# Optimization experiments

Hardware: AMD Instinct MI355X
Metric: run time of the kernel (lower is better)

Reference implementation:

```python
import jax, jax.numpy as jnp
import numpy as np

HIDDEN = 1024
HEADS = 16
HEAD_DIM = HIDDEN // HEADS  # 64
MLP_HIDDEN = int(HIDDEN * 4.0)  # 4096
B, L = 2, 2048
EPS_LN = 1e-6
EPS_RMS = 1e-6


def setup_inputs() -> dict:
    key = jax.random.key(0)
    ks = jax.random.split(key, 12)
    s = 0.02
    return {
        "x": jax.random.normal(ks[0], (B, L, HIDDEN), jnp.float32),
        "vec": jax.random.normal(ks[1], (B, HIDDEN), jnp.float32),
        "pe": jax.random.normal(ks[2], (1, 1, L, HEAD_DIM // 2, 2, 2), jnp.float32),
        "w_mod": jax.random.normal(ks[3], (HIDDEN, 3 * HIDDEN), jnp.float32) * s,
        "b_mod": jnp.zeros((3 * HIDDEN,), jnp.float32),
        "w1": jax.random.normal(ks[4], (HIDDEN, 3 * HIDDEN + MLP_HIDDEN), jnp.float32) * s,
        "b1": jnp.zeros((3 * HIDDEN + MLP_HIDDEN,), jnp.float32),
        "w_mlp": jax.random.normal(ks[5], (MLP_HIDDEN, HIDDEN), jnp.float32) * s,
        "b_mlp": jnp.zeros((HIDDEN,), jnp.float32),
        "w2": jax.random.normal(ks[6], (2 * HIDDEN, HIDDEN), jnp.float32) * s,
        "b2": jnp.zeros((HIDDEN,), jnp.float32),
        "q_scale": jnp.ones((HEAD_DIM,), jnp.float32),
        "k_scale": jnp.ones((HEAD_DIM,), jnp.float32),
    }


def _layernorm(x, eps=EPS_LN):
    m = jnp.mean(x, axis=-1, keepdims=True)
    v = jnp.mean(jnp.square(x - m), axis=-1, keepdims=True)
    return (x - m) * jax.lax.rsqrt(v + eps)


def _rmsnorm(x, scale, eps=EPS_RMS):
    rrms = jax.lax.rsqrt(jnp.mean(jnp.square(x), axis=-1, keepdims=True) + eps)
    return x * rrms * scale


def _apply_rope(t, pe):
    # t: [B,H,L,D]; pe: [1,1,L,D//2,2,2]
    t_ = t.reshape(*t.shape[:-1], -1, 1, 2)  # [B,H,L,D//2,1,2]
    out = pe[..., 0] * t_[..., 0] + pe[..., 1] * t_[..., 1]  # [B,H,L,D//2,2]
    return out.reshape(t.shape)


def reference(x, vec, pe, w_mod, b_mod, w1, b1, w_mlp, b_mlp, w2, b2, q_scale, k_scale):
    # adaLN modulation: silu(vec) -> Dense(3*dim) -> shift, scale, gate
    mod = (jax.nn.silu(vec) @ w_mod + b_mod)[:, None, :]  # [B,1,3H]
    shift, scale, gate = jnp.split(mod, 3, axis=-1)
    x_mod = (1.0 + scale) * _layernorm(x) + shift
    # fused QKV + MLP projection
    h = x_mod @ w1 + b1  # [B,L,3H+MH]
    qkv, mlp = h[..., : 3 * HIDDEN], h[..., 3 * HIDDEN :]
    qkv = qkv.reshape(x.shape[0], x.shape[1], 3, HEADS, HEAD_DIM)
    qkv = jnp.transpose(qkv, (2, 0, 3, 1, 4))  # [3,B,H,L,D]
    q, k, v = qkv[0], qkv[1], qkv[2]
    # QK-RMSNorm per head-dim
    q = _rmsnorm(q, q_scale)
    k = _rmsnorm(k, k_scale)
    # RoPE
    q = _apply_rope(q, pe)
    k = _apply_rope(k, pe)
    # attention
    scores = jnp.einsum("bhqd,bhkd->bhqk", q, k) * (HEAD_DIM ** -0.5)
    probs = jax.nn.softmax(scores, axis=-1)
    attn = jnp.einsum("bhqk,bhkd->bhqd", probs, v)
    attn = jnp.transpose(attn, (0, 2, 1, 3)).reshape(x.shape[0], x.shape[1], HIDDEN)
    # mlp branch (Dense with tanh activation per source) + fused output proj
    mlp_out = jnp.tanh(mlp @ w_mlp + b_mlp)
    out = jnp.concatenate([attn, mlp_out], axis=-1) @ w2 + b2
    return x + gate * out
```

## Files before the change

kernel.cpp:

```cpp
#include <hip/hip_runtime.h>
#include <stdint.h>


#define HID  1024
#define NH   16
#define HD   64
#define MLP  4096
#define D1   7168
#define DQKV 3072
#define DCAT 2048
#define BB   2
#define LL   2048
#define TOK  4096

typedef __attribute__((ext_vector_type(8))) short    bf16x8;
typedef __attribute__((ext_vector_type(4))) float    f32x4;
typedef __attribute__((ext_vector_type(4))) unsigned int u32x4;

__device__ __forceinline__ float b2f(unsigned short u) {
    unsigned int v = ((unsigned int)u) << 16;
    float f; __builtin_memcpy(&f, &v, 4); return f;
}
__device__ __forceinline__ unsigned short f2b(float f) {
    unsigned int v; __builtin_memcpy(&v, &f, 4);
    unsigned int r = (v + 0x7FFFu + ((v >> 16) & 1u)) >> 16;
    return (unsigned short)r;
}
__device__ __forceinline__ unsigned int pkbf2(float a, float b) {
    unsigned int ua, ub;
    __builtin_memcpy(&ua, &a, 4); __builtin_memcpy(&ub, &b, 4);
    return ((ua + 0x8000u) >> 16) | ((ub + 0x8000u) & 0xFFFF0000u);
}
__device__ __forceinline__ void gl_lds16(const unsigned short* g, unsigned short* l) {
    __builtin_amdgcn_global_load_lds(
        (const __attribute__((address_space(1))) unsigned int*)(g),
        (__attribute__((address_space(3))) unsigned int*)(l), 16, 0, 0);
}

__global__ void k_transpose_cvt(const float* __restrict__ in,
                                unsigned short* __restrict__ out, int R, int C) {
    __shared__ float tile[32][33];
    int bx = blockIdx.x, by = blockIdx.y;
    int tx = threadIdx.x, ty = threadIdx.y;
    #pragma unroll
    for (int i = 0; i < 4; i++) {
        int r = by * 32 + ty + i * 8;
        int c = bx * 32 + tx;
        tile[ty + i * 8][tx] = in[(size_t)r * C + c];
    }
    __syncthreads();
    #pragma unroll
    for (int i = 0; i < 4; i++) {
        int ro = bx * 32 + ty + i * 8;
        int co = by * 32 + tx;
        out[(size_t)ro * R + co] = f2b(tile[tx][ty + i * 8]);
    }
}

__global__ void k_mod(const float* __restrict__ vec,
                      const float* __restrict__ w_mod,
                      const float* __restrict__ b_mod,
                      float* __restrict__ mod) {
    __shared__ float sv[HID];
    __shared__ float red[8][32];
    int b = blockIdx.y, t = threadIdx.x;
    for (int j = t; j < HID; j += 256) {
        float v = vec[b * HID + j];
        sv[j] = v / (1.0f + __expf(-v));
    }
    __syncthreads();
    int n0 = blockIdx.x * 32;
    int on = t & 31, ks = t >> 5;
    float acc = 0.f;
    const float* wp = w_mod + (size_t)(ks * 128) * 3072 + n0 + on;
    #pragma unroll 4
    for (int k = 0; k < 128; k++) acc += sv[ks * 128 + k] * wp[(size_t)k * 3072];
    red[ks][on] = acc;
    __syncthreads();
    if (t < 32) {
        float s = 0.f;
        #pragma unroll
        for (int i = 0; i < 8; i++) s += red[i][t];
        mod[b * 3072 + n0 + t] = s + b_mod[n0 + t];
    }
}

__global__ void k_lnmod(const float* __restrict__ x,
                        const float* __restrict__ mod,
                        unsigned short* __restrict__ xmod) {
    int tok = blockIdx.x;
    int t = threadIdx.x;
    int b = tok >> 11;
    float4 v4 = *(const float4*)(x + (size_t)tok * HID + t * 4);
    float v0 = v4.x, v1 = v4.y, v2 = v4.z, v3 = v4.w;
    float s  = v0 + v1 + v2 + v3;
    float sq = v0*v0 + v1*v1 + v2*v2 + v3*v3;
    for (int off = 1; off < 64; off <<= 1) {
        s  += __shfl_xor(s,  off);
        sq += __shfl_xor(sq, off);
    }
    __shared__ float ls[4], lq[4];
    int w = t >> 6;
    if ((t & 63) == 0) { ls[w] = s; lq[w] = sq; }
    __syncthreads();
    s  = ls[0] + ls[1] + ls[2] + ls[3];
    sq = lq[0] + lq[1] + lq[2] + lq[3];
    float mean = s * (1.0f / HID);
    float var  = sq * (1.0f / HID) - mean * mean;
    float rstd = rsqrtf(var + 1e-6f);
    const float* mb = mod + b * 3072;
    float y[4] = {v0, v1, v2, v3};
    unsigned short r[4];
    #pragma unroll
    for (int j = 0; j < 4; j++) {
        int col = t * 4 + j;
        float nval = (y[j] - mean) * rstd;
        r[j] = f2b((1.0f + mb[1024 + col]) * nval + mb[col]);
    }
    unsigned int o0 = (unsigned int)r[0] | ((unsigned int)r[1] << 16);
    unsigned int o1 = (unsigned int)r[2] | ((unsigned int)r[3] << 16);
    *(uint2*)(xmod + (size_t)tok * HID + t * 4) = make_uint2(o0, o1);
}

template<int EPI>
__global__ __launch_bounds__(256) void k_gemm(
    const unsigned short* __restrict__ A, int lda,
    const unsigned short* __restrict__ Bt, int ldb,
    const float* __restrict__ bias,
    unsigned short* __restrict__ C, float* __restrict__ Cf, int ldc,
    int K,
    const float* __restrict__ xin,
    const float* __restrict__ mod) {
    __shared__ alignas(16) unsigned short As[128 * 64];
    __shared__ alignas(16) unsigned short Bs[128 * 64];
    int t = threadIdx.x;
    int bm = blockIdx.x, bn = blockIdx.y;
    int lane = t & 63, wave = t >> 6;
    int wm = (wave >> 1) * 64, wn = (wave & 1) * 64;
    int ln = lane & 15, kq = lane >> 4;
    int ln7 = ln & 7;

    f32x4 acc[4][4];
    #pragma unroll
    for (int i = 0; i < 4; i++)
        #pragma unroll
        for (int j = 0; j < 4; j++) acc[i][j] = {0.f, 0.f, 0.f, 0.f};

    int sr  = t >> 3;
    int scg = (t & 7) ^ (sr & 7);
    const unsigned short* Ab = A  + (size_t)(bm * 128) * lda;
    const unsigned short* Bb = Bt + (size_t)(bn * 128) * ldb;

    int ksplit = K / gridDim.z;
    int kbeg = blockIdx.z * ksplit, kend = kbeg + ksplit;

    for (int k0 = kbeg; k0 < kend; k0 += 64) {
        __syncthreads();
        #pragma unroll
        for (int c = 0; c < 4; c++) {
            gl_lds16(Ab + (size_t)(c * 32 + sr) * lda + k0 + scg * 8, &As[c * 2048 + t * 8]);
            gl_lds16(Bb + (size_t)(c * 32 + sr) * ldb + k0 + scg * 8, &Bs[c * 2048 + t * 8]);
        }
        __syncthreads();
        #pragma unroll
        for (int ks = 0; ks < 2; ks++) {
            int slot = ((ks * 4 + kq) ^ ln7) * 8;
            bf16x8 af[4], bfr[4];
            #pragma unroll
            for (int i = 0; i < 4; i++)
                af[i] = *(const bf16x8*)(&As[(wm + i * 16 + ln) * 64 + slot]);
            #pragma unroll
            for (int j = 0; j < 4; j++)
                bfr[j] = *(const bf16x8*)(&Bs[(wn + j * 16 + ln) * 64 + slot]);
            #pragma unroll
            for (int i = 0; i < 4; i++)
                #pragma unroll
                for (int j = 0; j < 4; j++)
                    acc[i][j] = __builtin_amdgcn_mfma_f32_16x16x32_bf16(af[i], bfr[j], acc[i][j], 0, 0, 0);
        }
    }

    #pragma unroll
    for (int i = 0; i < 4; i++) {
        #pragma unroll
        for (int j = 0; j < 4; j++) {
            int col = bn * 128 + wn + j * 16 + ln;
            float bv = (EPI == 3) ? 0.f : bias[col];
            #pragma unroll
            for (int r = 0; r < 4; r++) {
                int row = bm * 128 + wm + i * 16 + kq * 4 + r;
                float v = acc[i][j][r] + bv;
                if (EPI == 0) {
                    C[(size_t)row * ldc + col] = f2b(v);
                } else if (EPI == 1) {
                    C[(size_t)row * ldc + col] = f2b(tanhf(v));
                } else if (EPI == 2) {
                    int b = row >> 11;
                    Cf[(size_t)row * ldc + col] =
                        xin[(size_t)row * HID + col] + mod[b * 3072 + 2048 + col] * v;
                } else {
                    Cf[((size_t)blockIdx.z * TOK + row) * ldc + col] = v;
                }
            }
        }
    }
}

__global__ __launch_bounds__(256) void k_red1(const float* __restrict__ part,
                                              const float* __restrict__ bias,
                                              unsigned short* __restrict__ cat) {
    int idx = blockIdx.x * 256 + threadIdx.x;
    int row = idx >> 8;
    int c4  = (idx & 255) * 4;
    float4 p0 = *(const float4*)(part + (size_t)row * HID + c4);
    float4 p1 = *(const float4*)(part + ((size_t)TOK + row) * HID + c4);
    float4 bv = *(const float4*)(bias + c4);
    float a0 = tanhf(p0.x + p1.x + bv.x);
    float a1 = tanhf(p0.y + p1.y + bv.y);
    float a2 = tanhf(p0.z + p1.z + bv.z);
    float a3 = tanhf(p0.w + p1.w + bv.w);
    *(uint2*)(&cat[(size_t)row * DCAT + HID + c4]) =
        make_uint2(pkbf2(a0, a1), pkbf2(a2, a3));
}

__global__ __launch_bounds__(256) void k_red2(const float* __restrict__ part,
                                              const float* __restrict__ bias,
                                              const float* __restrict__ x,
                                              const float* __restrict__ mod,
                                              float* __restrict__ out) {
    int idx = blockIdx.x * 256 + threadIdx.x;
    int row = idx >> 8;
    int c4  = (idx & 255) * 4;
    int b = row >> 11;
    float4 p0 = *(const float4*)(part + (size_t)row * HID + c4);
    float4 p1 = *(const float4*)(part + ((size_t)TOK + row) * HID + c4);
    float4 bv = *(const float4*)(bias + c4);
    float4 gv = *(const float4*)(mod + b * 3072 + 2048 + c4);
    float4 xv = *(const float4*)(x + (size_t)row * HID + c4);
    float4 o;
    o.x = xv.x + gv.x * (p0.x + p1.x + bv.x);
    o.y = xv.y + gv.y * (p0.y + p1.y + bv.y);
    o.z = xv.z + gv.z * (p0.z + p1.z + bv.z);
    o.w = xv.w + gv.w * (p0.w + p1.w + bv.w);
    *(float4*)(out + (size_t)row * HID + c4) = o;
}

__global__ void k_qkrope(unsigned short* __restrict__ h,
                         const float* __restrict__ pe,
                         const float* __restrict__ q_scale,
                         const float* __restrict__ k_scale) {
    int tok = blockIdx.x;
    int l = tok & (LL - 1);
    int t = threadIdx.x;
    int lane = t & 63, wave = t >> 6;
    int hh = wave * 4 + (lane >> 4);
    int d0 = (lane & 15) * 4;
    unsigned short* row = h + (size_t)tok * D1;
    int i0 = d0 >> 1;
    const float* peb = pe + ((size_t)l * 32 + i0) * 4;
    float4 e0 = *(const float4*)(peb);
    float4 e1 = *(const float4*)(peb + 4);
    #pragma unroll
    for (int qk = 0; qk < 2; qk++) {
        unsigned short* p = row + qk * HID + hh * HD + d0;
        const float* sc = (qk == 0 ? q_scale : k_scale) + d0;
        uint2 qv = *(const uint2*)p;
        float v0 = b2f((unsigned short)(qv.x & 0xFFFF)), v1 = b2f((unsigned short)(qv.x >> 16));
        float v2 = b2f((unsigned short)(qv.y & 0xFFFF)), v3 = b2f((unsigned short)(qv.y >> 16));
        float ssq = v0*v0 + v1*v1 + v2*v2 + v3*v3;
        ssq += __shfl_xor(ssq, 1, 16);
        ssq += __shfl_xor(ssq, 2, 16);
        ssq += __shfl_xor(ssq, 4, 16);
        ssq += __shfl_xor(ssq, 8, 16);
        float rr = rsqrtf(ssq * (1.0f / HD) + 1e-6f);
        if (qk == 0) rr *= 0.18033688011112042f;
        v0 *= rr * sc[0];
        v1 *= rr * sc[1];
        v2 *= rr * sc[2];
        v3 *= rr * sc[3];
        float o0 = e0.x*v0 + e0.y*v1;
        float o1 = e0.z*v0 + e0.w*v1;
        float o2 = e1.x*v2 + e1.y*v3;
        float o3 = e1.z*v2 + e1.w*v3;
        *(uint2*)p = make_uint2(pkbf2(o0, o1), pkbf2(o2, o3));
    }
}

#define KT 64
#define LDP 72
__global__ __launch_bounds__(256) void k_attn(const unsigned short* __restrict__ h,
                                              unsigned short* __restrict__ cat) {
    __shared__ unsigned short Ks[KT * LDP];
    __shared__ unsigned short Vt[HD * LDP];
    __shared__ unsigned short Ps[4 * 16 * LDP];
    int t = threadIdx.x;
    int bx = blockIdx.x;
    int bh = blockIdx.y;
    int b = bh >> 4, hh = bh & 15;
    int lane = t & 63, w = t >> 6;
    int ln = lane & 15, quad = lane >> 4;
    const unsigned short* hb = h + (size_t)b * LL * D1;

    bf16x8 qf[2];
    {
        const unsigned short* qbase = hb + (size_t)(bx * 64 + w * 16) * D1 + hh * HD;
        #pragma unroll
        for (int ks = 0; ks < 2; ks++)
            qf[ks] = *(const bf16x8*)(qbase + (size_t)ln * D1 + ks * 32 + quad * 8);
    }

    f32x4 O[4];
    #pragma unroll
    for (int vn = 0; vn < 4; vn++) O[vn] = {0.f, 0.f, 0.f, 0.f};
    float m_ = -1e30f, l_ = 0.f;

    unsigned short* Psw = Ps + w * 16 * LDP;

    int skey = t >> 2, sdc = (t & 3) * 16;
    int p2 = (t & 31) * 2, db = (t >> 5) * 8;

    for (int kb = 0; kb < LL / KT; kb++) {
        __syncthreads();
        {
            const unsigned short* kbase = hb + (size_t)(kb * KT) * D1 + HID + hh * HD;
            u32x4 ka = *(const u32x4*)(kbase + (size_t)skey * D1 + sdc);
            u32x4 kc = *(const u32x4*)(kbase + (size_t)skey * D1 + sdc + 8);
            *(u32x4*)(&Ks[skey * LDP + sdc]) = ka;
            *(u32x4*)(&Ks[skey * LDP + sdc + 8]) = kc;
            const unsigned short* vbase = hb + (size_t)(kb * KT) * D1 + 2 * HID + hh * HD;
            u32x4 va = *(const u32x4*)(vbase + (size_t)p2 * D1 + db);
            u32x4 vb = *(const u32x4*)(vbase + (size_t)(p2 + 1) * D1 + db);
            #pragma unroll
            for (int j = 0; j < 8; j++) {
                unsigned int lo = (j & 1) ? (va[j >> 1] >> 16) : (va[j >> 1] & 0xFFFFu);
                unsigned int hi = (j & 1) ? (vb[j >> 1] >> 16) : (vb[j >> 1] & 0xFFFFu);
                *(unsigned int*)(&Vt[(db + j) * LDP + p2]) = lo | (hi << 16);
            }
        }
        __syncthreads();

        f32x4 st[4];
        #pragma unroll
        for (int kt = 0; kt < 4; kt++) {
            st[kt] = {0.f, 0.f, 0.f, 0.f};
            #pragma unroll
            for (int ks = 0; ks < 2; ks++) {
                bf16x8 kf = *(const bf16x8*)(&Ks[(kt * 16 + ln) * LDP + ks * 32 + quad * 8]);
                st[kt] = __builtin_amdgcn_mfma_f32_16x16x32_bf16(kf, qf[ks], st[kt], 0, 0, 0);
            }
        }

        {
            float p[16];
            float mx = -1e30f;
            #pragma unroll
            for (int kt = 0; kt < 4; kt++)
                #pragma unroll
                for (int r = 0; r < 4; r++) {
                    float v = st[kt][r];
                    p[kt * 4 + r] = v;
                    mx = fmaxf(mx, v);
                }
            mx = fmaxf(mx, __shfl_xor(mx, 16));
            mx = fmaxf(mx, __shfl_xor(mx, 32));
            float mnew = fmaxf(m_, mx);
            float alpha = __builtin_amdgcn_exp2f(m_ - mnew);
            m_ = mnew;
            float sum = 0.f;
            #pragma unroll
            for (int i = 0; i < 16; i++) {
                float e = __builtin_amdgcn_exp2f(p[i] - mnew);
                p[i] = e;
                sum += e;
            }
            sum += __shfl_xor(sum, 16);
            sum += __shfl_xor(sum, 32);
            l_ = l_ * alpha + sum;
            #pragma unroll
            for (int vn = 0; vn < 4; vn++)
                #pragma unroll
                for (int r = 0; r < 4; r++) O[vn][r] *= alpha;
            #pragma unroll
            for (int kt = 0; kt < 4; kt++) {
                unsigned long long pk =
                    (unsigned long long)pkbf2(p[kt*4+0], p[kt*4+1])
                  | ((unsigned long long)pkbf2(p[kt*4+2], p[kt*4+3]) << 32);
                *(unsigned long long*)(&Psw[ln * LDP + kt * 16 + quad * 4]) = pk;
            }
        }

        #pragma unroll
        for (int kt2 = 0; kt2 < 2; kt2++) {
            bf16x8 pb = *(const bf16x8*)(&Psw[ln * LDP + kt2 * 32 + quad * 8]);
            #pragma unroll
            for (int vn = 0; vn < 4; vn++) {
                bf16x8 vf = *(const bf16x8*)(&Vt[(vn * 16 + ln) * LDP + kt2 * 32 + quad * 8]);
                O[vn] = __builtin_amdgcn_mfma_f32_16x16x32_bf16(vf, pb, O[vn], 0, 0, 0);
            }
        }
    }

    {
        float rl = 1.0f / l_;
        size_t row = (size_t)(b * LL + bx * 64 + w * 16 + ln);
        #pragma unroll
        for (int vn = 0; vn < 4; vn++) {
            #pragma unroll
            for (int r2 = 0; r2 < 4; r2 += 2) {
                unsigned int pk = pkbf2(O[vn][r2] * rl, O[vn][r2 + 1] * rl);
                *(unsigned int*)(&cat[row * DCAT + hh * HD + vn * 16 + quad * 4 + r2]) = pk;
            }
        }
    }
}

extern "C" void kernel_launch(void* const* d_in, const int* in_sizes, int n_in,
                              void* d_out, int out_size, void* d_ws, size_t ws_size,
                              hipStream_t stream) {
    const float* x       = (const float*)d_in[0];
    const float* vec     = (const float*)d_in[1];
    const float* pe      = (const float*)d_in[2];
    const float* w_mod   = (const float*)d_in[3];
    const float* b_mod   = (const float*)d_in[4];
    const float* w1      = (const float*)d_in[5];
    const float* b1      = (const float*)d_in[6];
    const float* w_mlp   = (const float*)d_in[7];
    const float* b_mlp   = (const float*)d_in[8];
    const float* w2      = (const float*)d_in[9];
    const float* b2      = (const float*)d_in[10];
    const float* q_scale = (const float*)d_in[11];
    const float* k_scale = (const float*)d_in[12];
    float* out = (float*)d_out;

    char* ws = (char*)d_ws;
    size_t off = 0;
    float* mod = (float*)(ws + off);                     off += 6144 * 4;
    unsigned short* xmod  = (unsigned short*)(ws + off); off += (size_t)TOK * HID * 2;
    unsigned short* h     = (unsigned short*)(ws + off); off += (size_t)TOK * D1 * 2;
    unsigned short* cat   = (unsigned short*)(ws + off); off += (size_t)TOK * DCAT * 2;
    unsigned short* w1T   = (unsigned short*)(ws + off); off += (size_t)D1 * HID * 2;
    unsigned short* wmlpT = (unsigned short*)(ws + off); off += (size_t)HID * MLP * 2;
    unsigned short* w2T   = (unsigned short*)(ws + off); off += (size_t)HID * DCAT * 2;
    float* part = (float*)(ws + off);                    off += (size_t)2 * TOK * HID * 4;

    k_transpose_cvt<<<dim3(D1 / 32, HID / 32), dim3(32, 8), 0, stream>>>(w1, w1T, HID, D1);
    k_transpose_cvt<<<dim3(HID / 32, MLP / 32), dim3(32, 8), 0, stream>>>(w_mlp, wmlpT, MLP, HID);
    k_transpose_cvt<<<dim3(HID / 32, DCAT / 32), dim3(32, 8), 0, stream>>>(w2, w2T, DCAT, HID);

    k_mod<<<dim3(96, BB), 256, 0, stream>>>(vec, w_mod, b_mod, mod);
    k_lnmod<<<TOK, 256, 0, stream>>>(x, mod, xmod);

    k_gemm<0><<<dim3(TOK / 128, D1 / 128), 256, 0, stream>>>(
        xmod, HID, w1T, HID, b1, h, nullptr, D1, HID, nullptr, nullptr);

    k_qkrope<<<TOK, 256, 0, stream>>>(h, pe, q_scale, k_scale);

    k_attn<<<dim3(LL / 64, BB * NH), 256, 0, stream>>>(h, cat);

    k_gemm<3><<<dim3(TOK / 128, HID / 128, 2), 256, 0, stream>>>(
        h + DQKV, D1, wmlpT, MLP, b_mlp, nullptr, part, HID, MLP, nullptr, nullptr);
    k_red1<<<TOK * HID / 1024, 256, 0, stream>>>(part, b_mlp, cat);

    k_gemm<3><<<dim3(TOK / 128, HID / 128, 2), 256, 0, stream>>>(
        cat, DCAT, w2T, DCAT, b2, nullptr, part, HID, DCAT, nullptr, nullptr);
    k_red2<<<TOK * HID / 1024, 256, 0, stream>>>(part, b2, x, mod, out);
}
```

Measured before the change: 418.0 us.

## Pre-transpose V, use direct-to-LDS loads in attention, vectorize GEMM epilogue

Adds a kernel that transposes V into a per-head [D,L] buffer, so attention can stream K and V tiles with global-to-LDS 16-byte loads into XOR-swizzled shared memory. This replaces the register-level V transpose done in every block. The GEMM swaps its MFMA operands so each lane holds four consecutive output columns, which allows float4 and packed bf16 stores. It also remaps block indices into groups of 8 N-tiles to improve L2 reuse. The cost is an extra kernel launch plus an extra write and read of the V buffer.

After: 440.2 us. +5.3%, slower.

```diff
diff --git a/kernel.cpp b/kernel.cpp
--- a/kernel.cpp
+++ b/kernel.cpp
@@ -55,6 +55,25 @@
         int co = by * 32 + tx;
         out[(size_t)ro * R + co] = f2b(tile[tx][ty + i * 8]);
     }
+}
+
+__global__ void k_vt(const unsigned short* __restrict__ h,
+                     unsigned short* __restrict__ vT) {
+    __shared__ unsigned short tile[32][33];
+    int l0 = blockIdx.x * 32;
+    int d0 = (blockIdx.y & 1) * 32;
+    int bh = blockIdx.y >> 1;
+    int b = bh >> 4, hh = bh & 15;
+    int tx = threadIdx.x, ty = threadIdx.y;
+    const unsigned short* src = h + ((size_t)(b * LL) + l0) * D1 + 2 * HID + hh * HD + d0;
+    #pragma unroll
+    for (int i = 0; i < 4; i++)
+        tile[ty + i * 8][tx] = src[(size_t)(ty + i * 8) * D1 + tx];
+    __syncthreads();
+    unsigned short* dst = vT + ((size_t)(b * NH + hh) * HD + d0) * LL + l0;
+    #pragma unroll
+    for (int i = 0; i < 4; i++)
+        dst[(size_t)(ty + i * 8) * LL + tx] = tile[tx][ty + i * 8];
 }
 
 __global__ void k_mod(const float* __restrict__ vec,
@@ -134,10 +153,14 @@
     __shared__ alignas(16) unsigned short As[128 * 64];
     __shared__ alignas(16) unsigned short Bs[128 * 64];
     int t = threadIdx.x;
-    int bm = blockIdx.x, bn = blockIdx.y;
+    int bi = blockIdx.y * gridDim.x + blockIdx.x;
+    int span = gridDim.x * 8;
+    int pid = bi / span, rem = bi % span;
+    int bn = pid * 8 + (rem & 7);
+    int bm = rem >> 3;
     int lane = t & 63, wave = t >> 6;
     int wm = (wave >> 1) * 64, wn = (wave & 1) * 64;
-    int ln = lane & 15, kq = lane >> 4;
+    int ln = lane & 15, quad = lane >> 4;
     int ln7 = ln & 7;
 
     f32x4 acc[4][4];
@@ -164,7 +187,7 @@
         __syncthreads();
         #pragma unroll
         for (int ks = 0; ks < 2; ks++) {
-            int slot = ((ks * 4 + kq) ^ ln7) * 8;
+            int slot = ((ks * 4 + quad) ^ ln7) * 8;
             bf16x8 af[4], bfr[4];
             #pragma unroll
             for (int i = 0; i < 4; i++)
@@ -176,7 +199,7 @@
             for (int i = 0; i < 4; i++)
                 #pragma unroll
                 for (int j = 0; j < 4; j++)
-                    acc[i][j] = __builtin_amdgcn_mfma_f32_16x16x32_bf16(af[i], bfr[j], acc[i][j], 0, 0, 0);
+                    acc[i][j] = __builtin_amdgcn_mfma_f32_16x16x32_bf16(bfr[j], af[i], acc[i][j], 0, 0, 0);
         }
     }
 
@@ -184,22 +207,26 @@
     for (int i = 0; i < 4; i++) {
         #pragma unroll
         for (int j = 0; j < 4; j++) {
-            int col = bn * 128 + wn + j * 16 + ln;
-            float bv = (EPI == 3) ? 0.f : bias[col];
-            #pragma unroll
-            for (int r = 0; r < 4; r++) {
-                int row = bm * 128 + wm + i * 16 + kq * 4 + r;
-                float v = acc[i][j][r] + bv;
-                if (EPI == 0) {
-                    C[(size_t)row * ldc + col] = f2b(v);
-                } else if (EPI == 1) {
-                    C[(size_t)row * ldc + col] = f2b(tanhf(v));
-                } else if (EPI == 2) {
-                    int b = row >> 11;
-                    Cf[(size_t)row * ldc + col] =
-                        xin[(size_t)row * HID + col] + mod[b * 3072 + 2048 + col] * v;
+            int trow = bm * 128 + wm + i * 16 + ln;
+            int ncol = bn * 128 + wn + j * 16 + quad * 4;
+            f32x4 a = acc[i][j];
+            if (EPI == 3) {
+                float4 o = make_float4(a[0], a[1], a[2], a[3]);
+                *(float4*)(&Cf[((size_t)blockIdx.z * TOK + trow) * ldc + ncol]) = o;
+            } else {
+                float4 bv = *(const float4*)(bias + ncol);
+                float v0 = a[0] + bv.x, v1 = a[1] + bv.y, v2 = a[2] + bv.z, v3 = a[3] + bv.w;
+                if (EPI == 1) { v0 = tanhf(v0); v1 = tanhf(v1); v2 = tanhf(v2); v3 = tanhf(v3); }
+                if (EPI == 0 || EPI == 1) {
+                    *(uint2*)(&C[(size_t)trow * ldc + ncol]) =
+                        make_uint2(pkbf2(v0, v1), pkbf2(v2, v3));
                 } else {
-                    Cf[((size_t)blockIdx.z * TOK + row) * ldc + col] = v;
+                    int b = trow >> 11;
+                    float4 gv = *(const float4*)(mod + b * 3072 + 2048 + ncol);
+                    float4 xv = *(const float4*)(xin + (size_t)trow * HID + ncol);
+                    float4 o = make_float4(xv.x + gv.x * v0, xv.y + gv.y * v1,
+                                           xv.z + gv.z * v2, xv.w + gv.w * v3);
+                    *(float4*)(&Cf[(size_t)trow * ldc + ncol]) = o;
                 }
             }
         }
@@ -289,9 +316,10 @@
 #define KT 64
 #define LDP 72
 __global__ __launch_bounds__(256) void k_attn(const unsigned short* __restrict__ h,
+                                              const unsigned short* __restrict__ vT,
                                               unsigned short* __restrict__ cat) {
-    __shared__ unsigned short Ks[KT * LDP];
-    __shared__ unsigned short Vt[HD * LDP];
+    __shared__ alignas(16) unsigned short Ks[KT * 64];
+    __shared__ alignas(16) unsigned short Vs[HD * 64];
     __shared__ unsigned short Ps[4 * 16 * LDP];
     int t = threadIdx.x;
     int bx = blockIdx.x;
@@ -299,7 +327,9 @@
     int b = bh >> 4, hh = bh & 15;
     int lane = t & 63, w = t >> 6;
     int ln = lane & 15, quad = lane >> 4;
+    int ln7 = ln & 7;
     const unsigned short* hb = h + (size_t)b * LL * D1;
+    const unsigned short* vtb = vT + ((size_t)(b * NH + hh) * HD) * LL;
 
     bf16x8 qf[2];
     {
@@ -316,26 +346,18 @@
 
     unsigned short* Psw = Ps + w * 16 * LDP;
 
-    int skey = t >> 2, sdc = (t & 3) * 16;
-    int p2 = (t & 31) * 2, db = (t >> 5) * 8;
+    int srow = t >> 3;
+    int scg  = (t & 7) ^ (srow & 7);
 
     for (int kb = 0; kb < LL / KT; kb++) {
         __syncthreads();
         {
-            const unsigned short* kbase = hb + (size_t)(kb * KT) * D1 + HID + hh * HD;
-            u32x4 ka = *(const u32x4*)(kbase + (size_t)skey * D1 + sdc);
-            u32x4 kc = *(const u32x4*)(kbase + (size_t)skey * D1 + sdc + 8);
-            *(u32x4*)(&Ks[skey * LDP + sdc]) = ka;
-            *(u32x4*)(&Ks[skey * LDP + sdc + 8]) = kc;
-            const unsigned short* vbase = hb + (size_t)(kb * KT) * D1 + 2 * HID + hh * HD;
-            u32x4 va = *(const u32x4*)(vbase + (size_t)p2 * D1 + db);
-            u32x4 vb = *(const u32x4*)(vbase + (size_t)(p2 + 1) * D1 + db);
-            #pragma unroll
-            for (int j = 0; j < 8; j++) {
-                unsigned int lo = (j & 1) ? (va[j >> 1] >> 16) : (va[j >> 1] & 0xFFFFu);
-                unsigned int hi = (j & 1) ? (vb[j >> 1] >> 16) : (vb[j >> 1] & 0xFFFFu);
-                *(unsigned int*)(&Vt[(db + j) * LDP + p2]) = lo | (hi << 16);
-            }
+            const unsigned short* kb0 = hb + (size_t)(kb * KT) * D1 + HID + hh * HD;
+            gl_lds16(kb0 + (size_t)srow * D1 + scg * 8,        &Ks[t * 8]);
+            gl_lds16(kb0 + (size_t)(srow + 32) * D1 + scg * 8, &Ks[2048 + t * 8]);
+            const unsigned short* vb0 = vtb + kb * KT;
+            gl_lds16(vb0 + (size_t)srow * LL + scg * 8,        &Vs[t * 8]);
+            gl_lds16(vb0 + (size_t)(srow + 32) * LL + scg * 8, &Vs[2048 + t * 8]);
         }
         __syncthreads();
 
@@ -345,7 +367,7 @@
             st[kt] = {0.f, 0.f, 0.f, 0.f};
             #pragma unroll
             for (int ks = 0; ks < 2; ks++) {
-                bf16x8 kf = *(const bf16x8*)(&Ks[(kt * 16 + ln) * LDP + ks * 32 + quad * 8]);
+                bf16x8 kf = *(const bf16x8*)(&Ks[(kt * 16 + ln) * 64 + (((ks * 4 + quad) ^ ln7) * 8)]);
                 st[kt] = __builtin_amdgcn_mfma_f32_16x16x32_bf16(kf, qf[ks], st[kt], 0, 0, 0);
             }
         }
@@ -394,7 +416,7 @@
             bf16x8 pb = *(const bf16x8*)(&Psw[ln * LDP + kt2 * 32 + quad * 8]);
             #pragma unroll
             for (int vn = 0; vn < 4; vn++) {
-                bf16x8 vf = *(const bf16x8*)(&Vt[(vn * 16 + ln) * LDP + kt2 * 32 + quad * 8]);
+                bf16x8 vf = *(const bf16x8*)(&Vs[(vn * 16 + ln) * 64 + (((kt2 * 4 + quad) ^ ln7) * 8)]);
                 O[vn] = __builtin_amdgcn_mfma_f32_16x16x32_bf16(vf, pb, O[vn], 0, 0, 0);
             }
         }
@@ -441,6 +463,7 @@
     unsigned short* w1T   = (unsigned short*)(ws + off); off += (size_t)D1 * HID * 2;
     unsigned short* wmlpT = (unsigned short*)(ws + off); off += (size_t)HID * MLP * 2;
     unsigned short* w2T   = (unsigned short*)(ws + off); off += (size_t)HID * DCAT * 2;
+    unsigned short* vTr   = (unsigned short*)(ws + off); off += (size_t)BB * NH * HD * LL * 2;
     float* part = (float*)(ws + off);                    off += (size_t)2 * TOK * HID * 4;
 
     k_transpose_cvt<<<dim3(D1 / 32, HID / 32), dim3(32, 8), 0, stream>>>(w1, w1T, HID, D1);
@@ -453,9 +476,10 @@
     k_gemm<0><<<dim3(TOK / 128, D1 / 128), 256, 0, stream>>>(
         xmod, HID, w1T, HID, b1, h, nullptr, D1, HID, nullptr, nullptr);
 
+    k_vt<<<dim3(LL / 32, 2 * BB * NH), dim3(32, 8), 0, stream>>>(h, vTr);
     k_qkrope<<<TOK, 256, 0, stream>>>(h, pe, q_scale, k_scale);
 
-    k_attn<<<dim3(LL / 64, BB * NH), 256, 0, stream>>>(h, cat);
+    k_attn<<<dim3(LL / 64, BB * NH), 256, 0, stream>>>(h, vTr, cat);
 
     k_gemm<3><<<dim3(TOK / 128, HID / 128, 2), 256, 0, stream>>>(
         h + DQKV, D1, wmlpT, MLP, b_mlp, nullptr, part, HID, MLP, nullptr, nullptr);
```
